# Kernel tuning notes

Measured on AMD Instinct MI355X. Metric: run time of the kernel, lower is better.

## Reference

```python
import jax, jax.numpy as jnp
import numpy as np

N_NODES = 100000
N_EDGES = 800000
NUM_GRAPHS = 512
IN_DIM = 16
EDGE_DIM = 1
HID = 64       # emb_dim
MLP_H = 32     # hidden_layers inside each MPNNLayer
L = 3          # num_layers
EPS = 1e-5


def setup_inputs() -> dict:
    key = jax.random.key(0)
    ks = jax.random.split(key, 24)
    s = 0.05
    inp = {
        "x": jax.random.normal(ks[0], (N_NODES, IN_DIM), jnp.float32),
        "edge_index": jax.random.randint(ks[1], (2, N_EDGES), 0, N_NODES),
        "edge_attr": jax.random.uniform(ks[2], (N_EDGES, EDGE_DIM), jnp.float32),
        "batch": jnp.sort(jax.random.randint(ks[3], (N_NODES,), 0, NUM_GRAPHS)),
        # input projection
        "lin_in_w": jax.random.normal(ks[4], (IN_DIM, HID), jnp.float32) * s,
        "lin_in_b": jnp.zeros((HID,), jnp.float32),
        # message MLP (stacked over L layers): Linear(129->32), BN(32), ReLU, Linear(32->64), ReLU, BN(64)
        "msg_w1": jax.random.normal(ks[5], (L, 2 * HID + EDGE_DIM, MLP_H), jnp.float32) * s,
        "msg_b1": jnp.zeros((L, MLP_H), jnp.float32),
        "msg_g1": jnp.ones((L, MLP_H), jnp.float32),
        "msg_be1": jnp.zeros((L, MLP_H), jnp.float32),
        "msg_w2": jax.random.normal(ks[6], (L, MLP_H, HID), jnp.float32) * s,
        "msg_b2": jnp.zeros((L, HID), jnp.float32),
        "msg_g2": jnp.ones((L, HID), jnp.float32),
        "msg_be2": jnp.zeros((L, HID), jnp.float32),
        # update MLP: Linear(128->32), BN(32), ReLU, Linear(32->64), ReLU, BN(64)
        "upd_w1": jax.random.normal(ks[7], (L, 2 * HID, MLP_H), jnp.float32) * s,
        "upd_b1": jnp.zeros((L, MLP_H), jnp.float32),
        "upd_g1": jnp.ones((L, MLP_H), jnp.float32),
        "upd_be1": jnp.zeros((L, MLP_H), jnp.float32),
        "upd_w2": jax.random.normal(ks[8], (L, MLP_H, HID), jnp.float32) * s,
        "upd_b2": jnp.zeros((L, HID), jnp.float32),
        "upd_g2": jnp.ones((L, HID), jnp.float32),
        "upd_be2": jnp.zeros((L, HID), jnp.float32),
        # head Linear(64->1) + ReLU
        "out_w": jax.random.normal(ks[9], (HID, 1), jnp.float32) * s,
        "out_b": jnp.zeros((1,), jnp.float32),
    }
    return inp


def _bn(h, g, b):
    # BatchNorm1d, training-mode batch stats (biased variance), dropout treated as identity (eval)
    mu = jnp.mean(h, axis=0)
    var = jnp.var(h, axis=0)
    return g * (h - mu) * jax.lax.rsqrt(var + EPS) + b


def reference(x, edge_index, edge_attr, batch,
              lin_in_w, lin_in_b,
              msg_w1, msg_b1, msg_g1, msg_be1, msg_w2, msg_b2, msg_g2, msg_be2,
              upd_w1, upd_b1, upd_g1, upd_be1, upd_w2, upd_b2, upd_g2, upd_be2,
              out_w, out_b):
    src = edge_index[0]  # x_j source
    dst = edge_index[1]  # x_i target / aggregation index
    h = x @ lin_in_w + lin_in_b  # [N, HID]
    for l in range(L):
        # message: cat([x_i, x_j, edge_attr]) -> Linear -> BN -> ReLU -> Linear -> ReLU -> BN
        m_in = jnp.concatenate([h[dst], h[src], edge_attr], axis=1)  # [E, 2*HID+EDGE_DIM]
        m = jax.nn.relu(_bn(m_in @ msg_w1[l] + msg_b1[l], msg_g1[l], msg_be1[l]))
        m = _bn(jax.nn.relu(m @ msg_w2[l] + msg_b2[l]), msg_g2[l], msg_be2[l])
        # aggregate: scatter-add over destination nodes
        agg = jax.ops.segment_sum(m, dst, num_segments=N_NODES)  # [N, HID]
        # update: cat([x, aggr]) -> Linear -> BN -> ReLU -> Linear -> ReLU -> BN
        u_in = jnp.concatenate([h, agg], axis=1)  # [N, 2*HID]
        u = jax.nn.relu(_bn(u_in @ upd_w1[l] + upd_b1[l], upd_g1[l], upd_be1[l]))
        u = _bn(jax.nn.relu(u @ upd_w2[l] + upd_b2[l]), upd_g2[l], upd_be2[l])
        h = h + u  # residual (x += conv(...))
    # global mean pool
    pooled = jax.ops.segment_sum(h, batch, num_segments=NUM_GRAPHS)
    counts = jax.ops.segment_sum(jnp.ones((h.shape[0],), h.dtype), batch, num_segments=NUM_GRAPHS)
    pooled = pooled / jnp.maximum(counts, 1.0)[:, None]
    return jax.nn.relu(pooled @ out_w + out_b).reshape(-1)  # [NUM_GRAPHS]
```

## Files before the change

### kernel.cpp

```cpp
#include <hip/hip_runtime.h>
#include <hip/hip_bf16.h>

#define N_NODES   100000
#define N_EDGES   800000
#define NUM_GRAPHS 512
#define IN_DIM    16
#define HID       64
#define MLP_H     32
#define EPS       1e-5f
#define TPB       256
#define SCAN_B    1024
#define NCHUNK    ((N_NODES + SCAN_B - 1) / SCAN_B)
#define GSB       2048
#define NWAVES    (GSB * 4)
#define PER_W     ((N_EDGES + NWAVES - 1) / NWAVES)

using nh2   = decltype(__builtin_amdgcn_cvt_pkrtz(0.f, 0.f));
typedef _Float16 f16x8 __attribute__((ext_vector_type(8)));
typedef float    f32x4 __attribute__((ext_vector_type(4)));
typedef int      i32x4 __attribute__((ext_vector_type(4)));

__device__ __forceinline__ nh2 pack2(float a, float b) {
  return __builtin_amdgcn_cvt_pkrtz(a, b);
}
__device__ __forceinline__ float wsum(float v) {
  v += __shfl_xor(v, 1, 64);
  v += __shfl_xor(v, 2, 64);
  v += __shfl_xor(v, 4, 64);
  v += __shfl_xor(v, 8, 64);
  v += __shfl_xor(v, 16, 64);
  v += __shfl_xor(v, 32, 64);
  return v;
}
__device__ __forceinline__ int lbound(const int* __restrict__ rs, int key) {
  int lo = 0, hi = N_NODES;
  while (lo < hi) { int m = (lo + hi) >> 1; if (rs[m] < key) lo = m + 1; else hi = m; }
  return lo;
}

__global__ __launch_bounds__(TPB) void k_deg(const int* __restrict__ ei, int* __restrict__ deg) {
  int e = blockIdx.x * TPB + threadIdx.x;
  if (e < N_EDGES) atomicAdd(&deg[ei[N_EDGES + e]], 1);
}

__global__ __launch_bounds__(SCAN_B) void k_scan_part(const int* __restrict__ deg,
                                                      int* __restrict__ partials) {
  __shared__ int red[SCAN_B];
  int i = blockIdx.x * SCAN_B + threadIdx.x;
  red[threadIdx.x] = (i < N_NODES) ? deg[i] : 0;
  __syncthreads();
  for (int off = SCAN_B / 2; off > 0; off >>= 1) {
    if (threadIdx.x < off) red[threadIdx.x] += red[threadIdx.x + off];
    __syncthreads();
  }
  if (threadIdx.x == 0) partials[blockIdx.x] = red[0];
}

__global__ void k_scan_mid(int* __restrict__ partials, int* __restrict__ row_start) {
  int run = 0;
  for (int b = 0; b < NCHUNK; ++b) { int t = partials[b]; partials[b] = run; run += t; }
  row_start[N_NODES] = run;
}

__global__ __launch_bounds__(SCAN_B) void k_scan_fin(const int* __restrict__ deg,
                                                     const int* __restrict__ partials,
                                                     int* __restrict__ row_start,
                                                     int* __restrict__ cursor) {
  __shared__ int buf[2][SCAN_B];
  int t = threadIdx.x, i = blockIdx.x * SCAN_B + t;
  int v = (i < N_NODES) ? deg[i] : 0;
  buf[0][t] = v;
  __syncthreads();
  int cur = 0;
  for (int off = 1; off < SCAN_B; off <<= 1) {
    int nv = buf[cur][t] + ((t >= off) ? buf[cur][t - off] : 0);
    buf[cur ^ 1][t] = nv; cur ^= 1;
    __syncthreads();
  }
  if (i < N_NODES) {
    int excl = buf[cur][t] - v + partials[blockIdx.x];
    row_start[i] = excl;
    cursor[i] = excl;
  }
}

__global__ __launch_bounds__(TPB) void k_fill(const int* __restrict__ ei,
                                              const float* __restrict__ ea,
                                              int* __restrict__ cursor,
                                              int* __restrict__ srcS,
                                              int* __restrict__ dstS,
                                              float* __restrict__ eaS) {
  int e = blockIdx.x * TPB + threadIdx.x;
  if (e >= N_EDGES) return;
  int dst = ei[N_EDGES + e];
  int pos = atomicAdd(&cursor[dst], 1);
  srcS[pos] = ei[e];
  dstS[pos] = dst;
  eaS[pos] = ea[e];
}

__global__ __launch_bounds__(TPB) void k_lin_in(const float* __restrict__ x,
                                                const float* __restrict__ w,
                                                const float* __restrict__ b,
                                                float* __restrict__ h) {
  int i = blockIdx.x * TPB + threadIdx.x;
  if (i >= N_NODES) return;
  float xi[IN_DIM];
  const float4* xp = reinterpret_cast<const float4*>(x + i * IN_DIM);
#pragma unroll
  for (int q = 0; q < 4; ++q) {
    float4 v = xp[q];
    xi[4*q] = v.x; xi[4*q+1] = v.y; xi[4*q+2] = v.z; xi[4*q+3] = v.w;
  }
  float4* hp = reinterpret_cast<float4*>(h + i * HID);
#pragma unroll
  for (int j4 = 0; j4 < HID/4; ++j4) {
    float o[4];
#pragma unroll
    for (int c = 0; c < 4; ++c) {
      int j = j4*4 + c;
      float acc = b[j];
#pragma unroll
      for (int k = 0; k < IN_DIM; ++k) acc += xi[k] * w[k*HID + j];
      o[c] = acc;
    }
    float4 ov = {o[0], o[1], o[2], o[3]};
    hp[j4] = ov;
  }
}

__global__ __launch_bounds__(TPB) void k_pq(const float* __restrict__ h,
                                            const float* __restrict__ w1,
                                            const float* __restrict__ b1,
                                            float* __restrict__ P,
                                            float* __restrict__ Q) {
  int i = blockIdx.x * TPB + threadIdx.x;
  if (i >= N_NODES) return;
  float p[MLP_H], q[MLP_H];
#pragma unroll
  for (int j = 0; j < MLP_H; ++j) { p[j] = b1[j]; q[j] = 0.f; }
  const float4* hp = reinterpret_cast<const float4*>(h + i * HID);
#pragma unroll 2
  for (int k4 = 0; k4 < 16; ++k4) {
    float4 a = hp[k4];
    const float* wp = w1 + (k4*4) * MLP_H;
    const float* wq = w1 + (64 + k4*4) * MLP_H;
#pragma unroll
    for (int j = 0; j < MLP_H; ++j) {
      p[j] += a.x*wp[j] + a.y*wp[MLP_H+j] + a.z*wp[2*MLP_H+j] + a.w*wp[3*MLP_H+j];
      q[j] += a.x*wq[j] + a.y*wq[MLP_H+j] + a.z*wq[2*MLP_H+j] + a.w*wq[3*MLP_H+j];
    }
  }
  float4* pp = reinterpret_cast<float4*>(P + i * MLP_H);
  float4* qp = reinterpret_cast<float4*>(Q + i * MLP_H);
#pragma unroll
  for (int c = 0; c < MLP_H/4; ++c) {
    float4 pv = {p[4*c], p[4*c+1], p[4*c+2], p[4*c+3]};
    float4 qv = {q[4*c], q[4*c+1], q[4*c+2], q[4*c+3]};
    pp[c] = pv; qp[c] = qv;
  }
}

__global__ __launch_bounds__(TPB) void k_gather(const float* __restrict__ P,
                                                const float* __restrict__ Q,
                                                const int* __restrict__ srcS,
                                                const int* __restrict__ dstS,
                                                const float* __restrict__ eaS,
                                                const float* __restrict__ w1,
                                                _Float16* __restrict__ z1h,
                                                float* __restrict__ gstat) {
  const int lane = threadIdx.x & 63;
  const int k = lane & 31;
  const int half = lane >> 5;
  const float weak = w1[128 * MLP_H + k];
  float s = 0.f, q = 0.f;
  const int wv = blockIdx.x * 4 + (threadIdx.x >> 6);
  const int c0 = wv * PER_W;
  const int c1 = min(c0 + PER_W, N_EDGES);
  if (c0 < N_EDGES) {
    const int rounds = (c1 - c0 + 1) >> 1;
    const int e0 = c0 + half;
    int ea0 = min(e0, c1 - 1);
    int ea1 = min(e0 + 2, c1 - 1);
    float aA = eaS[ea0], aB = eaS[ea1];
    float qA = Q[srcS[ea0] * MLP_H + k], qB = Q[srcS[ea1] * MLP_H + k];
    float pA = P[dstS[ea0] * MLP_H + k], pB = P[dstS[ea1] * MLP_H + k];
    for (int r = 0; r < rounds; ++r) {
      const int ecur = e0 + 2 * r;
      const bool vc = ecur < c1;
      const int ecl = min(ecur, c1 - 1);
      float z = pA + qA + aA * weak;
      pA = pB; qA = qB; aA = aB;
      const int en = min(e0 + 2 * (r + 2), c1 - 1);
      aB = eaS[en]; qB = Q[srcS[en] * MLP_H + k]; pB = P[dstS[en] * MLP_H + k];
      if (vc) {
        z1h[ecl * MLP_H + k] = (_Float16)z;
        s += z; q = fmaf(z, z, q);
      }
    }
  }
  s += __shfl_xor(s, 32, 64);
  q += __shfl_xor(q, 32, 64);
  __shared__ float ls[4][MLP_H], lq[4][MLP_H];
  const int w = threadIdx.x >> 6;
  if (lane < MLP_H) { ls[w][lane] = s; lq[w][lane] = q; }
  __syncthreads();
  const int t = threadIdx.x;
  if (t < MLP_H)
    unsafeAtomicAdd(&gstat[t], ls[0][t] + ls[1][t] + ls[2][t] + ls[3][t]);
  else if (t < 2*MLP_H)
    unsafeAtomicAdd(&gstat[t], lq[0][t-MLP_H] + lq[1][t-MLP_H] + lq[2][t-MLP_H] + lq[3][t-MLP_H]);
}

__global__ __launch_bounds__(TPB) void k_msgdot(const _Float16* __restrict__ z1h,
                                                const int* __restrict__ rs,
                                                const float* __restrict__ gstat_in,
                                                const float* __restrict__ g1,
                                                const float* __restrict__ be1,
                                                const float* __restrict__ w2,
                                                const float* __restrict__ b2,
                                                float* __restrict__ agg,
                                                float* __restrict__ gstat_out) {
  const int lane = threadIdx.x & 63;
  const int col = lane & 15;
  const int g   = lane >> 4;
  float a1v[8], c1v[8];
#pragma unroll
  for (int i = 0; i < 8; ++i) {
    int kf = g*8 + i;
    float mu = gstat_in[kf] * (1.f / N_EDGES);
    float var = fmaxf(gstat_in[MLP_H + kf] * (1.f / N_EDGES) - mu * mu, 0.f);
    float a = g1[kf] * rsqrtf(var + EPS);
    a1v[i] = a; c1v[i] = be1[kf] - a * mu;
  }
  f16x8 bf0, bf1, bf2, bf3;
#define MKB(BF, C) { i32x4 bw; \
  _Pragma("unroll") for (int ii = 0; ii < 4; ++ii) { \
    nh2 p = pack2(w2[(g*8 + 2*ii) * HID + (C)*16 + col], \
                  w2[(g*8 + 2*ii + 1) * HID + (C)*16 + col]); \
    bw[ii] = __builtin_bit_cast(int, p); } \
  BF = __builtin_bit_cast(f16x8, bw); }
  MKB(bf0, 0) MKB(bf1, 1) MKB(bf2, 2) MKB(bf3, 3)
#undef MKB
  float b2c[4];
#pragma unroll
  for (int c = 0; c < 4; ++c) b2c[c] = b2[c*16 + col];

  float sacc[4] = {0.f,0.f,0.f,0.f}, qacc[4] = {0.f,0.f,0.f,0.f};
  const int wv = blockIdx.x * 4 + (threadIdx.x >> 6);
  const int key0 = min(wv * PER_W, N_EDGES);
  const int key1 = min((wv + 1) * PER_W, N_EDGES);
  const int n0 = lbound(rs, key0);
  const int n1 = (wv == NWAVES - 1) ? N_NODES : lbound(rs, key1);

  for (int n = n0; n < n1; ++n) {
    const int start = rs[n], end = rs[n + 1];
    float aggacc[4] = {0.f,0.f,0.f,0.f};
    for (int t0 = start; t0 < end; t0 += 16) {
      const int ec = min(t0 + col, end - 1);
      f16x8 zv = *reinterpret_cast<const f16x8*>(z1h + ec * MLP_H + g * 8);
      i32x4 aw;
#pragma unroll
      for (int i = 0; i < 4; ++i) {
        float m0 = fmaxf(fmaf(a1v[2*i],   (float)zv[2*i],   c1v[2*i]),   0.f);
        float m1 = fmaxf(fmaf(a1v[2*i+1], (float)zv[2*i+1], c1v[2*i+1]), 0.f);
        aw[i] = __builtin_bit_cast(int, pack2(m0, m1));
      }
      f16x8 af = __builtin_bit_cast(f16x8, aw);
      f32x4 zc = {0.f,0.f,0.f,0.f};
      f32x4 cc0 = __builtin_amdgcn_mfma_f32_16x16x32_f16(af, bf0, zc, 0, 0, 0);
      f32x4 cc1 = __builtin_amdgcn_mfma_f32_16x16x32_f16(af, bf1, zc, 0, 0, 0);
      f32x4 cc2 = __builtin_amdgcn_mfma_f32_16x16x32_f16(af, bf2, zc, 0, 0, 0);
      f32x4 cc3 = __builtin_amdgcn_mfma_f32_16x16x32_f16(af, bf3, zc, 0, 0, 0);
      bool vld[4];
#pragma unroll
      for (int reg = 0; reg < 4; ++reg) vld[reg] = (t0 + g*4 + reg) < end;
#define EPI(CC, CI) { \
  _Pragma("unroll") for (int reg = 0; reg < 4; ++reg) { \
    float tv = fmaxf(CC[reg] + b2c[CI], 0.f); \
    tv = vld[reg] ? tv : 0.f; \
    aggacc[CI] += tv; qacc[CI] = fmaf(tv, tv, qacc[CI]); } }
      EPI(cc0, 0) EPI(cc1, 1) EPI(cc2, 2) EPI(cc3, 3)
#undef EPI
    }
#pragma unroll
    for (int c = 0; c < 4; ++c) sacc[c] += aggacc[c];
#pragma unroll
    for (int c = 0; c < 4; ++c) {
      aggacc[c] += __shfl_xor(aggacc[c], 16, 64);
      aggacc[c] += __shfl_xor(aggacc[c], 32, 64);
    }
    float aout = (g == 0) ? aggacc[0] : (g == 1) ? aggacc[1] : (g == 2) ? aggacc[2] : aggacc[3];
    agg[n * HID + g * 16 + col] = aout;
  }
#pragma unroll
  for (int c = 0; c < 4; ++c) {
    sacc[c] += __shfl_xor(sacc[c], 16, 64);
    sacc[c] += __shfl_xor(sacc[c], 32, 64);
    qacc[c] += __shfl_xor(qacc[c], 16, 64);
    qacc[c] += __shfl_xor(qacc[c], 32, 64);
  }
  __shared__ float ls[4][HID], lq[4][HID];
  const int w = threadIdx.x >> 6;
  if (g == 0) {
#pragma unroll
    for (int c = 0; c < 4; ++c) { ls[w][c*16 + col] = sacc[c]; lq[w][c*16 + col] = qacc[c]; }
  }
  __syncthreads();
  const int t = threadIdx.x;
  if (t < HID)
    unsafeAtomicAdd(&gstat_out[t], ls[0][t] + ls[1][t] + ls[2][t] + ls[3][t]);
  else if (t < 2*HID)
    unsafeAtomicAdd(&gstat_out[t], lq[0][t-HID] + lq[1][t-HID] + lq[2][t-HID] + lq[3][t-HID]);
}

__global__ __launch_bounds__(TPB) void k_upd1(const float* __restrict__ h,
                                              const float* __restrict__ agg,
                                              const int* __restrict__ deg,
                                              const float* __restrict__ gstat_in,
                                              const float* __restrict__ g2,
                                              const float* __restrict__ be2,
                                              const float* __restrict__ w1,
                                              const float* __restrict__ b1,
                                              float* __restrict__ zu1,
                                              float* __restrict__ gstat_out) {
  __shared__ float sa[HID], sc[HID];
  {
    int t = threadIdx.x;
    if (t < HID) {
      float mu = gstat_in[t] * (1.f / N_EDGES);
      float var = fmaxf(gstat_in[HID + t] * (1.f / N_EDGES) - mu * mu, 0.f);
      float a = g2[t] * rsqrtf(var + EPS);
      sa[t] = a; sc[t] = be2[t] - a * mu;
    }
  }
  __syncthreads();
  int i = blockIdx.x * TPB + threadIdx.x;
  bool valid = i < N_NODES;
  float acc[MLP_H];
#pragma unroll
  for (int j = 0; j < MLP_H; ++j) acc[j] = 0.f;
  if (valid) {
#pragma unroll
    for (int j = 0; j < MLP_H; ++j) acc[j] = b1[j];
    const float4* hp = reinterpret_cast<const float4*>(h + i * HID);
#pragma unroll 2
    for (int k4 = 0; k4 < 16; ++k4) {
      float4 a = hp[k4];
      const float* wr = w1 + (k4*4) * MLP_H;
#pragma unroll
      for (int j = 0; j < MLP_H; ++j)
        acc[j] += a.x*wr[j] + a.y*wr[MLP_H+j] + a.z*wr[2*MLP_H+j] + a.w*wr[3*MLP_H+j];
    }
    float degf = (float)deg[i];
    const float4* ap = reinterpret_cast<const float4*>(agg + i * HID);
#pragma unroll 2
    for (int k4 = 0; k4 < 16; ++k4) {
      float4 g4 = ap[k4];
      int k = k4*4;
      float a0 = sa[k]  *g4.x + sc[k]  *degf;
      float a1 = sa[k+1]*g4.y + sc[k+1]*degf;
      float a2 = sa[k+2]*g4.z + sc[k+2]*degf;
      float a3 = sa[k+3]*g4.w + sc[k+3]*degf;
      const float* wr = w1 + (64 + k) * MLP_H;
#pragma unroll
      for (int j = 0; j < MLP_H; ++j)
        acc[j] += a0*wr[j] + a1*wr[MLP_H+j] + a2*wr[2*MLP_H+j] + a3*wr[3*MLP_H+j];
    }
    float4* zp = reinterpret_cast<float4*>(zu1 + i * MLP_H);
#pragma unroll
    for (int c = 0; c < MLP_H/4; ++c) {
      float4 o = {acc[4*c], acc[4*c+1], acc[4*c+2], acc[4*c+3]};
      zp[c] = o;
    }
  }
  int lane = threadIdx.x & 63;
  float ks = 0.f, kq = 0.f;
#pragma unroll
  for (int j = 0; j < MLP_H; ++j) {
    float sv = wsum(acc[j]);
    float qv = wsum(acc[j]*acc[j]);
    if (lane == j) { ks = sv; kq = qv; }
  }
  __shared__ float ls[4][MLP_H], lq[4][MLP_H];
  int w = threadIdx.x >> 6;
  if (lane < MLP_H) { ls[w][lane] = ks; lq[w][lane] = kq; }
  __syncthreads();
  int t = threadIdx.x;
  if (t < MLP_H)
    unsafeAtomicAdd(&gstat_out[t], ls[0][t] + ls[1][t] + ls[2][t] + ls[3][t]);
  else if (t < 2*MLP_H)
    unsafeAtomicAdd(&gstat_out[t], lq[0][t-MLP_H] + lq[1][t-MLP_H] + lq[2][t-MLP_H] + lq[3][t-MLP_H]);
}

__global__ __launch_bounds__(TPB) void k_upd2(const float* __restrict__ zu1,
                                              const float* __restrict__ gstat_in,
                                              const float* __restrict__ gu1,
                                              const float* __restrict__ beu1,
                                              const float* __restrict__ w2,
                                              const float* __restrict__ b2,
                                              float* __restrict__ tu,
                                              float* __restrict__ gstat_out) {
  __shared__ float sa[MLP_H], sc[MLP_H];
  {
    int t = threadIdx.x;
    if (t < MLP_H) {
      float mu = gstat_in[t] * (1.f / N_NODES);
      float var = fmaxf(gstat_in[MLP_H + t] * (1.f / N_NODES) - mu * mu, 0.f);
      float a = gu1[t] * rsqrtf(var + EPS);
      sa[t] = a; sc[t] = beu1[t] - a * mu;
    }
  }
  __syncthreads();
  int i = blockIdx.x * TPB + threadIdx.x;
  bool valid = i < N_NODES;
  float m1[MLP_H];
#pragma unroll
  for (int kk = 0; kk < MLP_H; ++kk) m1[kk] = 0.f;
  if (valid) {
    const float4* zp = reinterpret_cast<const float4*>(zu1 + i * MLP_H);
#pragma unroll
    for (int c = 0; c < MLP_H/4; ++c) {
      float4 z = zp[c];
      int kk = 4*c;
      m1[kk]   = fmaxf(sa[kk]  *z.x + sc[kk],   0.f);
      m1[kk+1] = fmaxf(sa[kk+1]*z.y + sc[kk+1], 0.f);
      m1[kk+2] = fmaxf(sa[kk+2]*z.z + sc[kk+2], 0.f);
      m1[kk+3] = fmaxf(sa[kk+3]*z.w + sc[kk+3], 0.f);
    }
  }
  int lane = threadIdx.x & 63;
  float ks = 0.f, kq = 0.f;
#pragma unroll 2
  for (int j4 = 0; j4 < HID/4; ++j4) {
    float tv[4];
#pragma unroll
    for (int c = 0; c < 4; ++c) {
      int j = j4*4 + c;
      float v = 0.f;
      if (valid) {
        v = b2[j];
#pragma unroll
        for (int kk = 0; kk < MLP_H; ++kk) v += m1[kk] * w2[kk*HID + j];
        v = fmaxf(v, 0.f);
      }
      tv[c] = v;
      float sv = wsum(v);
      float qv = wsum(v*v);
      if (lane == j) { ks = sv; kq = qv; }
    }
    if (valid) {
      float4 o = {tv[0], tv[1], tv[2], tv[3]};
      *reinterpret_cast<float4*>(tu + i * HID + j4*4) = o;
    }
  }
  __shared__ float ls[4][HID], lq[4][HID];
  int w = threadIdx.x >> 6;
  ls[w][lane] = ks; lq[w][lane] = kq;
  __syncthreads();
  int t = threadIdx.x;
  if (t < HID)
    unsafeAtomicAdd(&gstat_out[t], ls[0][t] + ls[1][t] + ls[2][t] + ls[3][t]);
  else if (t < 2*HID)
    unsafeAtomicAdd(&gstat_out[t], lq[0][t-HID] + lq[1][t-HID] + lq[2][t-HID] + lq[3][t-HID]);
}

__global__ __launch_bounds__(TPB) void k_resid(float* __restrict__ h,
                                               const float* __restrict__ tu,
                                               const float* __restrict__ gstat_in,
                                               const float* __restrict__ gu2,
                                               const float* __restrict__ beu2) {
  __shared__ float sa[HID], sc[HID];
  {
    int t = threadIdx.x;
    if (t < HID) {
      float mu = gstat_in[t] * (1.f / N_NODES);
      float var = fmaxf(gstat_in[HID + t] * (1.f / N_NODES) - mu * mu, 0.f);
      float a = gu2[t] * rsqrtf(var + EPS);
      sa[t] = a; sc[t] = beu2[t] - a * mu;
    }
  }
  __syncthreads();
  int idx = blockIdx.x * TPB + threadIdx.x;
  if (idx >= N_NODES * (HID/4)) return;
  int j0 = (idx & (HID/4 - 1)) * 4;
  float4 hv = reinterpret_cast<const float4*>(h)[idx];
  float4 tv = reinterpret_cast<const float4*>(tu)[idx];
  hv.x += sa[j0]  *tv.x + sc[j0];
  hv.y += sa[j0+1]*tv.y + sc[j0+1];
  hv.z += sa[j0+2]*tv.z + sc[j0+2];
  hv.w += sa[j0+3]*tv.w + sc[j0+3];
  reinterpret_cast<float4*>(h)[idx] = hv;
}

__global__ __launch_bounds__(TPB) void k_pool_head(const float* __restrict__ h,
                                                   const int* __restrict__ batch,
                                                   const float* __restrict__ ow,
                                                   const float* __restrict__ ob,
                                                   float* __restrict__ out) {
  int g = blockIdx.x;
  int lo = 0, hi = N_NODES;
  while (lo < hi) { int mid = (lo+hi) >> 1; if (batch[mid] < g) lo = mid+1; else hi = mid; }
  int start = lo;
  lo = start; hi = N_NODES;
  while (lo < hi) { int mid = (lo+hi) >> 1; if (batch[mid] < g+1) lo = mid+1; else hi = mid; }
  int end = lo;
  int j = threadIdx.x & 63;
  int sub = threadIdx.x >> 6;
  float acc = 0.f;
  for (int n = start + sub; n < end; n += 4) acc += h[n*HID + j];
  __shared__ float red[TPB];
  red[threadIdx.x] = acc;
  __syncthreads();
  if (threadIdx.x < 64) {
    float s = red[threadIdx.x] + red[64+threadIdx.x] + red[128+threadIdx.x] + red[192+threadIdx.x];
    float cnt = (float)(end - start);
    float pooled = s / fmaxf(cnt, 1.0f);
    float v = pooled * ow[threadIdx.x];
    v = wsum(v);
    if (threadIdx.x == 0) out[g] = fmaxf(v + ob[0], 0.f);
  }
}

extern "C" void kernel_launch(void* const* d_in, const int* in_sizes, int n_in,
                              void* d_out, int out_size, void* d_ws, size_t ws_size,
                              hipStream_t stream) {
  const float* x       = (const float*)d_in[0];
  const int*   ei      = (const int*)  d_in[1];
  const float* ea      = (const float*)d_in[2];
  const int*   batch   = (const int*)  d_in[3];
  const float* lin_w   = (const float*)d_in[4];
  const float* lin_b   = (const float*)d_in[5];
  const float* msg_w1  = (const float*)d_in[6];
  const float* msg_b1  = (const float*)d_in[7];
  const float* msg_g1  = (const float*)d_in[8];
  const float* msg_be1 = (const float*)d_in[9];
  const float* msg_w2  = (const float*)d_in[10];
  const float* msg_b2  = (const float*)d_in[11];
  const float* msg_g2  = (const float*)d_in[12];
  const float* msg_be2 = (const float*)d_in[13];
  const float* upd_w1  = (const float*)d_in[14];
  const float* upd_b1  = (const float*)d_in[15];
  const float* upd_g1  = (const float*)d_in[16];
  const float* upd_be1 = (const float*)d_in[17];
  const float* upd_w2  = (const float*)d_in[18];
  const float* upd_b2  = (const float*)d_in[19];
  const float* upd_g2  = (const float*)d_in[20];
  const float* upd_be2 = (const float*)d_in[21];
  const float* out_w   = (const float*)d_in[22];
  const float* out_b   = (const float*)d_in[23];
  float* out = (float*)d_out;

  float* W     = (float*)d_ws;
  float* h     = W;
  float* P     = W + 6400000;
  float* Qb    = W + 9600000;
  float* agg   = W + 12800000;
  float* z1    = W + 19200000;
  _Float16* z1h = (_Float16*)z1;
  float* zu1   = z1 + 12800000;
  float* tu    = z1 + 16000000;
  float* eaS   = W + 44800000;
  float* stats = W + 45600000;
  int*   ib    = (int*)(W + 45601152);
  int* deg       = ib;
  int* row_start = ib + 100000;
  int* cursor    = ib + 200001;
  int* srcS      = ib + 300001;
  int* dstS      = ib + 1100001;
  int* partials  = ib + 1900001;

  hipMemsetAsync(stats, 0, 3*384*sizeof(float), stream);
  hipMemsetAsync(deg, 0, N_NODES*sizeof(int), stream);

  k_deg<<<N_EDGES/TPB, TPB, 0, stream>>>(ei, deg);
  k_scan_part<<<NCHUNK, SCAN_B, 0, stream>>>(deg, partials);
  k_scan_mid<<<1, 1, 0, stream>>>(partials, row_start);
  k_scan_fin<<<NCHUNK, SCAN_B, 0, stream>>>(deg, partials, row_start, cursor);
  k_fill<<<N_EDGES/TPB, TPB, 0, stream>>>(ei, ea, cursor, srcS, dstS, eaS);

  k_lin_in<<<(N_NODES+TPB-1)/TPB, TPB, 0, stream>>>(x, lin_w, lin_b, h);

  const int NODE_BLKS = (N_NODES + TPB - 1) / TPB;

  for (int l = 0; l < 3; ++l) {
    const float* mw1 = msg_w1 + (size_t)l*129*MLP_H;
    const float* mb1 = msg_b1 + l*MLP_H;
    const float* mg1 = msg_g1 + l*MLP_H;
    const float* mbe1= msg_be1 + l*MLP_H;
    const float* mw2 = msg_w2 + (size_t)l*MLP_H*HID;
    const float* mb2 = msg_b2 + l*HID;
    const float* mg2 = msg_g2 + l*HID;
    const float* mbe2= msg_be2 + l*HID;
    const float* uw1 = upd_w1 + (size_t)l*128*MLP_H;
    const float* ub1 = upd_b1 + l*MLP_H;
    const float* ug1 = upd_g1 + l*MLP_H;
    const float* ube1= upd_be1 + l*MLP_H;
    const float* uw2 = upd_w2 + (size_t)l*MLP_H*HID;
    const float* ub2 = upd_b2 + l*HID;
    const float* ug2 = upd_g2 + l*HID;
    const float* ube2= upd_be2 + l*HID;
    float* st = stats + l*384;

    k_pq<<<NODE_BLKS, TPB, 0, stream>>>(h, mw1, mb1, P, Qb);
    k_gather<<<GSB, TPB, 0, stream>>>(P, Qb, srcS, dstS, eaS, mw1, z1h, st);
    k_msgdot<<<GSB, TPB, 0, stream>>>(z1h, row_start, st, mg1, mbe1, mw2, mb2, agg, st+64);
    k_upd1<<<NODE_BLKS, TPB, 0, stream>>>(h, agg, deg, st+64, mg2, mbe2, uw1, ub1, zu1, st+192);
    k_upd2<<<NODE_BLKS, TPB, 0, stream>>>(zu1, st+192, ug1, ube1, uw2, ub2, tu, st+256);
    k_resid<<<(N_NODES*(HID/4)+TPB-1)/TPB, TPB, 0, stream>>>(h, tu, st+256, ug2, ube2);
  }

  k_pool_head<<<NUM_GRAPHS, TPB, 0, stream>>>(h, batch, out_w, out_b, out);
}
```

Baseline: 1.138 ms.

## Split node MLP kernels across waves, store Q in fp16, move BN stats to separate pass

```diff
diff --git a/kernel.cpp b/kernel.cpp
--- a/kernel.cpp
+++ b/kernel.cpp
@@ -14,6 +14,7 @@
 #define GSB       2048
 #define NWAVES    (GSB * 4)
 #define PER_W     ((N_EDGES + NWAVES - 1) / NWAVES)
+#define NODEBLKS  ((N_NODES + 63) / 64)
 
 using nh2   = decltype(__builtin_amdgcn_cvt_pkrtz(0.f, 0.f));
 typedef _Float16 f16x8 __attribute__((ext_vector_type(8)));
@@ -133,36 +134,48 @@
                                             const float* __restrict__ w1,
                                             const float* __restrict__ b1,
                                             float* __restrict__ P,
-                                            float* __restrict__ Q) {
-  int i = blockIdx.x * TPB + threadIdx.x;
+                                            _Float16* __restrict__ Qh) {
+  const int wave = blockIdx.x * 4 + (threadIdx.x >> 6);
+  const int lane = threadIdx.x & 63;
+  const int part = wave & 3;
+  const int i = (wave >> 2) * 64 + lane;
   if (i >= N_NODES) return;
-  float p[MLP_H], q[MLP_H];
-#pragma unroll
-  for (int j = 0; j < MLP_H; ++j) { p[j] = b1[j]; q[j] = 0.f; }
+  const int jb = (part & 1) * 16;
+  const bool isQ = part >= 2;
+  const float* wbase = w1 + (isQ ? 64 * MLP_H : 0) + jb;
+  float acc[16];
+#pragma unroll
+  for (int j = 0; j < 16; ++j) acc[j] = isQ ? 0.f : b1[jb + j];
   const float4* hp = reinterpret_cast<const float4*>(h + i * HID);
-#pragma unroll 2
+#pragma unroll 4
   for (int k4 = 0; k4 < 16; ++k4) {
     float4 a = hp[k4];
-    const float* wp = w1 + (k4*4) * MLP_H;
-    const float* wq = w1 + (64 + k4*4) * MLP_H;
-#pragma unroll
-    for (int j = 0; j < MLP_H; ++j) {
-      p[j] += a.x*wp[j] + a.y*wp[MLP_H+j] + a.z*wp[2*MLP_H+j] + a.w*wp[3*MLP_H+j];
-      q[j] += a.x*wq[j] + a.y*wq[MLP_H+j] + a.z*wq[2*MLP_H+j] + a.w*wq[3*MLP_H+j];
-    }
-  }
-  float4* pp = reinterpret_cast<float4*>(P + i * MLP_H);
-  float4* qp = reinterpret_cast<float4*>(Q + i * MLP_H);
-#pragma unroll
-  for (int c = 0; c < MLP_H/4; ++c) {
-    float4 pv = {p[4*c], p[4*c+1], p[4*c+2], p[4*c+3]};
-    float4 qv = {q[4*c], q[4*c+1], q[4*c+2], q[4*c+3]};
-    pp[c] = pv; qp[c] = qv;
+    const float* wr = wbase + (k4*4) * MLP_H;
+#pragma unroll
+    for (int j = 0; j < 16; ++j)
+      acc[j] += a.x*wr[j] + a.y*wr[MLP_H+j] + a.z*wr[2*MLP_H+j] + a.w*wr[3*MLP_H+j];
+  }
+  if (!isQ) {
+    float4* pp = reinterpret_cast<float4*>(P + i * MLP_H + jb);
+#pragma unroll
+    for (int c = 0; c < 4; ++c) {
+      float4 o = {acc[4*c], acc[4*c+1], acc[4*c+2], acc[4*c+3]};
+      pp[c] = o;
+    }
+  } else {
+    i32x4 o0, o1;
+#pragma unroll
+    for (int c = 0; c < 4; ++c) {
+      o0[c] = __builtin_bit_cast(int, pack2(acc[2*c],     acc[2*c+1]));
+      o1[c] = __builtin_bit_cast(int, pack2(acc[8+2*c],   acc[8+2*c+1]));
+    }
+    i32x4* qp = reinterpret_cast<i32x4*>(Qh + i * MLP_H + jb);
+    qp[0] = o0; qp[1] = o1;
   }
 }
 
 __global__ __launch_bounds__(TPB) void k_gather(const float* __restrict__ P,
-                                                const float* __restrict__ Q,
+                                                const _Float16* __restrict__ Qh,
                                                 const int* __restrict__ srcS,
                                                 const int* __restrict__ dstS,
                                                 const float* __restrict__ eaS,
@@ -183,7 +196,7 @@
     int ea0 = min(e0, c1 - 1);
     int ea1 = min(e0 + 2, c1 - 1);
     float aA = eaS[ea0], aB = eaS[ea1];
-    float qA = Q[srcS[ea0] * MLP_H + k], qB = Q[srcS[ea1] * MLP_H + k];
+    float qA = (float)Qh[srcS[ea0] * MLP_H + k], qB = (float)Qh[srcS[ea1] * MLP_H + k];
     float pA = P[dstS[ea0] * MLP_H + k], pB = P[dstS[ea1] * MLP_H + k];
     for (int r = 0; r < rounds; ++r) {
       const int ecur = e0 + 2 * r;
@@ -192,7 +205,7 @@
       float z = pA + qA + aA * weak;
       pA = pB; qA = qB; aA = aB;
       const int en = min(e0 + 2 * (r + 2), c1 - 1);
-      aB = eaS[en]; qB = Q[srcS[en] * MLP_H + k]; pB = P[dstS[en] * MLP_H + k];
+      aB = eaS[en]; qB = (float)Qh[srcS[en] * MLP_H + k]; pB = P[dstS[en] * MLP_H + k];
       if (vc) {
         z1h[ecl * MLP_H + k] = (_Float16)z;
         s += z; q = fmaf(z, z, q);
@@ -322,8 +335,7 @@
                                               const float* __restrict__ be2,
                                               const float* __restrict__ w1,
                                               const float* __restrict__ b1,
-                                              float* __restrict__ zu1,
-                                              float* __restrict__ gstat_out) {
+                                              float* __restrict__ zu1) {
   __shared__ float sa[HID], sc[HID];
   {
     int t = threadIdx.x;
@@ -335,62 +347,45 @@
     }
   }
   __syncthreads();
-  int i = blockIdx.x * TPB + threadIdx.x;
-  bool valid = i < N_NODES;
-  float acc[MLP_H];
-#pragma unroll
-  for (int j = 0; j < MLP_H; ++j) acc[j] = 0.f;
-  if (valid) {
-#pragma unroll
-    for (int j = 0; j < MLP_H; ++j) acc[j] = b1[j];
-    const float4* hp = reinterpret_cast<const float4*>(h + i * HID);
-#pragma unroll 2
-    for (int k4 = 0; k4 < 16; ++k4) {
-      float4 a = hp[k4];
-      const float* wr = w1 + (k4*4) * MLP_H;
-#pragma unroll
-      for (int j = 0; j < MLP_H; ++j)
-        acc[j] += a.x*wr[j] + a.y*wr[MLP_H+j] + a.z*wr[2*MLP_H+j] + a.w*wr[3*MLP_H+j];
-    }
-    float degf = (float)deg[i];
-    const float4* ap = reinterpret_cast<const float4*>(agg + i * HID);
-#pragma unroll 2
-    for (int k4 = 0; k4 < 16; ++k4) {
-      float4 g4 = ap[k4];
-      int k = k4*4;
-      float a0 = sa[k]  *g4.x + sc[k]  *degf;
-      float a1 = sa[k+1]*g4.y + sc[k+1]*degf;
-      float a2 = sa[k+2]*g4.z + sc[k+2]*degf;
-      float a3 = sa[k+3]*g4.w + sc[k+3]*degf;
-      const float* wr = w1 + (64 + k) * MLP_H;
-#pragma unroll
-      for (int j = 0; j < MLP_H; ++j)
-        acc[j] += a0*wr[j] + a1*wr[MLP_H+j] + a2*wr[2*MLP_H+j] + a3*wr[3*MLP_H+j];
-    }
-    float4* zp = reinterpret_cast<float4*>(zu1 + i * MLP_H);
-#pragma unroll
-    for (int c = 0; c < MLP_H/4; ++c) {
-      float4 o = {acc[4*c], acc[4*c+1], acc[4*c+2], acc[4*c+3]};
-      zp[c] = o;
-    }
-  }
-  int lane = threadIdx.x & 63;
-  float ks = 0.f, kq = 0.f;
-#pragma unroll
-  for (int j = 0; j < MLP_H; ++j) {
-    float sv = wsum(acc[j]);
-    float qv = wsum(acc[j]*acc[j]);
-    if (lane == j) { ks = sv; kq = qv; }
-  }
-  __shared__ float ls[4][MLP_H], lq[4][MLP_H];
-  int w = threadIdx.x >> 6;
-  if (lane < MLP_H) { ls[w][lane] = ks; lq[w][lane] = kq; }
-  __syncthreads();
-  int t = threadIdx.x;
-  if (t < MLP_H)
-    unsafeAtomicAdd(&gstat_out[t], ls[0][t] + ls[1][t] + ls[2][t] + ls[3][t]);
-  else if (t < 2*MLP_H)
-    unsafeAtomicAdd(&gstat_out[t], lq[0][t-MLP_H] + lq[1][t-MLP_H] + lq[2][t-MLP_H] + lq[3][t-MLP_H]);
+  const int wave = blockIdx.x * 4 + (threadIdx.x >> 6);
+  const int lane = threadIdx.x & 63;
+  const int part = wave & 1;
+  const int jb = part * 16;
+  const int i = (wave >> 1) * 64 + lane;
+  if (i >= N_NODES) return;
+  float acc[16];
+#pragma unroll
+  for (int j = 0; j < 16; ++j) acc[j] = b1[jb + j];
+  const float4* hp = reinterpret_cast<const float4*>(h + i * HID);
+#pragma unroll 4
+  for (int k4 = 0; k4 < 16; ++k4) {
+    float4 a = hp[k4];
+    const float* wr = w1 + (k4*4) * MLP_H + jb;
+#pragma unroll
+    for (int j = 0; j < 16; ++j)
+      acc[j] += a.x*wr[j] + a.y*wr[MLP_H+j] + a.z*wr[2*MLP_H+j] + a.w*wr[3*MLP_H+j];
+  }
+  float degf = (float)deg[i];
+  const float4* ap = reinterpret_cast<const float4*>(agg + i * HID);
+#pragma unroll 4
+  for (int k4 = 0; k4 < 16; ++k4) {
+    float4 g4 = ap[k4];
+    int k = k4*4;
+    float a0 = sa[k]  *g4.x + sc[k]  *degf;
+    float a1 = sa[k+1]*g4.y + sc[k+1]*degf;
+    float a2 = sa[k+2]*g4.z + sc[k+2]*degf;
+    float a3 = sa[k+3]*g4.w + sc[k+3]*degf;
+    const float* wr = w1 + (64 + k) * MLP_H + jb;
+#pragma unroll
+    for (int j = 0; j < 16; ++j)
+      acc[j] += a0*wr[j] + a1*wr[MLP_H+j] + a2*wr[2*MLP_H+j] + a3*wr[3*MLP_H+j];
+  }
+  float4* zp = reinterpret_cast<float4*>(zu1 + i * MLP_H + jb);
+#pragma unroll
+  for (int c = 0; c < 4; ++c) {
+    float4 o = {acc[4*c], acc[4*c+1], acc[4*c+2], acc[4*c+3]};
+    zp[c] = o;
+  }
 }
 
 __global__ __launch_bounds__(TPB) void k_upd2(const float* __restrict__ zu1,
@@ -399,8 +394,7 @@
                                               const float* __restrict__ beu1,
                                               const float* __restrict__ w2,
                                               const float* __restrict__ b2,
-                                              float* __restrict__ tu,
-                                              float* __restrict__ gstat_out) {
+                                              float* __restrict__ tu) {
   __shared__ float sa[MLP_H], sc[MLP_H];
   {
     int t = threadIdx.x;
@@ -412,57 +406,60 @@
     }
   }
   __syncthreads();
-  int i = blockIdx.x * TPB + threadIdx.x;
-  bool valid = i < N_NODES;
+  const int wave = blockIdx.x * 4 + (threadIdx.x >> 6);
+  const int lane = threadIdx.x & 63;
+  const int part = wave & 1;
+  const int jb = part * 32;
+  const int i = (wave >> 1) * 64 + lane;
+  if (i >= N_NODES) return;
   float m1[MLP_H];
-#pragma unroll
-  for (int kk = 0; kk < MLP_H; ++kk) m1[kk] = 0.f;
-  if (valid) {
-    const float4* zp = reinterpret_cast<const float4*>(zu1 + i * MLP_H);
-#pragma unroll
-    for (int c = 0; c < MLP_H/4; ++c) {
-      float4 z = zp[c];
-      int kk = 4*c;
-      m1[kk]   = fmaxf(sa[kk]  *z.x + sc[kk],   0.f);
-      m1[kk+1] = fmaxf(sa[kk+1]*z.y + sc[kk+1], 0.f);
-      m1[kk+2] = fmaxf(sa[kk+2]*z.z + sc[kk+2], 0.f);
-      m1[kk+3] = fmaxf(sa[kk+3]*z.w + sc[kk+3], 0.f);
-    }
-  }
-  int lane = threadIdx.x & 63;
-  float ks = 0.f, kq = 0.f;
-#pragma unroll 2
-  for (int j4 = 0; j4 < HID/4; ++j4) {
+  const float4* zp = reinterpret_cast<const float4*>(zu1 + i * MLP_H);
+#pragma unroll
+  for (int c = 0; c < MLP_H/4; ++c) {
+    float4 z = zp[c];
+    int kk = 4*c;
+    m1[kk]   = fmaxf(sa[kk]  *z.x + sc[kk],   0.f);
+    m1[kk+1] = fmaxf(sa[kk+1]*z.y + sc[kk+1], 0.f);
+    m1[kk+2] = fmaxf(sa[kk+2]*z.z + sc[kk+2], 0.f);
+    m1[kk+3] = fmaxf(sa[kk+3]*z.w + sc[kk+3], 0.f);
+  }
+#pragma unroll
+  for (int j4 = 0; j4 < 8; ++j4) {
     float tv[4];
 #pragma unroll
     for (int c = 0; c < 4; ++c) {
-      int j = j4*4 + c;
-      float v = 0.f;
-      if (valid) {
-        v = b2[j];
-#pragma unroll
-        for (int kk = 0; kk < MLP_H; ++kk) v += m1[kk] * w2[kk*HID + j];
-        v = fmaxf(v, 0.f);
-      }
-      tv[c] = v;
-      float sv = wsum(v);
-      float qv = wsum(v*v);
-      if (lane == j) { ks = sv; kq = qv; }
-    }
-    if (valid) {
-      float4 o = {tv[0], tv[1], tv[2], tv[3]};
-      *reinterpret_cast<float4*>(tu + i * HID + j4*4) = o;
-    }
-  }
-  __shared__ float ls[4][HID], lq[4][HID];
-  int w = threadIdx.x >> 6;
-  ls[w][lane] = ks; lq[w][lane] = kq;
-  __syncthreads();
-  int t = threadIdx.x;
-  if (t < HID)
-    unsafeAtomicAdd(&gstat_out[t], ls[0][t] + ls[1][t] + ls[2][t] + ls[3][t]);
-  else if (t < 2*HID)
-    unsafeAtomicAdd(&gstat_out[t], lq[0][t-HID] + lq[1][t-HID] + lq[2][t-HID] + lq[3][t-HID]);
+      int j = jb + j4*4 + c;
+      float v = b2[j];
+#pragma unroll
+      for (int kk = 0; kk < MLP_H; ++kk) v += m1[kk] * w2[kk*HID + j];
+      tv[c] = fmaxf(v, 0.f);
+    }
+    float4 o = {tv[0], tv[1], tv[2], tv[3]};
+    *reinterpret_cast<float4*>(tu + i * HID + jb + j4*4) = o;
+  }
+}
+
+template <int NF>
+__global__ __launch_bounds__(TPB) void k_colstats(const float* __restrict__ X,
+                                                  int nrows, float* __restrict__ gstat) {
+  const int RPB = TPB / NF;
+  int f = threadIdx.x % NF;
+  int rloc = threadIdx.x / NF;
+  float s = 0.f, q = 0.f;
+  for (int r = blockIdx.x * RPB + rloc; r < nrows; r += gridDim.x * RPB) {
+    float v = X[r * NF + f];
+    s += v; q = fmaf(v, v, q);
+  }
+  __shared__ float ls[TPB], lq[TPB];
+  ls[threadIdx.x] = s; lq[threadIdx.x] = q;
+  __syncthreads();
+  if (threadIdx.x < NF) {
+    float ss = 0.f, qq = 0.f;
+#pragma unroll
+    for (int r = 0; r < RPB; ++r) { ss += ls[r*NF + f]; qq += lq[r*NF + f]; }
+    unsafeAtomicAdd(&gstat[f], ss);
+    unsafeAtomicAdd(&gstat[NF + f], qq);
+  }
 }
 
 __global__ __launch_bounds__(TPB) void k_resid(float* __restrict__ h,
@@ -554,7 +551,7 @@
   float* W     = (float*)d_ws;
   float* h     = W;
   float* P     = W + 6400000;
-  float* Qb    = W + 9600000;
+  _Float16* Qh = (_Float16*)(W + 9600000);
   float* agg   = W + 12800000;
   float* z1    = W + 19200000;
   _Float16* z1h = (_Float16*)z1;
@@ -581,7 +578,8 @@
 
   k_lin_in<<<(N_NODES+TPB-1)/TPB, TPB, 0, stream>>>(x, lin_w, lin_b, h);
 
-  const int NODE_BLKS = (N_NODES + TPB - 1) / TPB;
+  const int PQ_BLKS   = NODEBLKS;
+  const int UPD_BLKS  = (2 * NODEBLKS + 3) / 4;
 
   for (int l = 0; l < 3; ++l) {
     const float* mw1 = msg_w1 + (size_t)l*129*MLP_H;
@@ -602,11 +600,13 @@
     const float* ube2= upd_be2 + l*HID;
     float* st = stats + l*384;
 
-    k_pq<<<NODE_BLKS, TPB, 0, stream>>>(h, mw1, mb1, P, Qb);
-    k_gather<<<GSB, TPB, 0, stream>>>(P, Qb, srcS, dstS, eaS, mw1, z1h, st);
+    k_pq<<<PQ_BLKS, TPB, 0, stream>>>(h, mw1, mb1, P, Qh);
+    k_gather<<<GSB, TPB, 0, stream>>>(P, Qh, srcS, dstS, eaS, mw1, z1h, st);
     k_msgdot<<<GSB, TPB, 0, stream>>>(z1h, row_start, st, mg1, mbe1, mw2, mb2, agg, st+64);
-    k_upd1<<<NODE_BLKS, TPB, 0, stream>>>(h, agg, deg, st+64, mg2, mbe2, uw1, ub1, zu1, st+192);
-    k_upd2<<<NODE_BLKS, TPB, 0, stream>>>(zu1, st+192, ug1, ube1, uw2, ub2, tu, st+256);
+    k_upd1<<<UPD_BLKS, TPB, 0, stream>>>(h, agg, deg, st+64, mg2, mbe2, uw1, ub1, zu1);
+    k_colstats<MLP_H><<<512, TPB, 0, stream>>>(zu1, N_NODES, st+192);
+    k_upd2<<<UPD_BLKS, TPB, 0, stream>>>(zu1, st+192, ug1, ube1, uw2, ub2, tu);
+    k_colstats<HID><<<512, TPB, 0, stream>>>(tu, N_NODES, st+256);
     k_resid<<<(N_NODES*(HID/4)+TPB-1)/TPB, TPB, 0, stream>>>(h, tu, st+256, ug2, ube2);
   }
 
```

Result: slower. 1.384 ms (+21.6%).
